# Performance work log

Hardware: AMD Instinct MI355X
Metric: run time of the kernel (lower is better)

Reference implementation:

```python
import jax, jax.numpy as jnp
import numpy as np

N, E, F_IN, F_OUT, K = 10000, 640000, 256, 64, 4


def setup_inputs() -> dict:
    key = jax.random.key(0)
    ks = jax.random.split(key, 8)
    feat = jax.random.normal(ks[0], (N, F_IN), dtype=jnp.float32)
    feat_a = jax.random.normal(ks[1], (N, F_IN), dtype=jnp.float32)
    edge_index = jax.random.randint(ks[2], (2, E), 0, N)
    graph_neigh = jax.random.uniform(ks[3], (N, N), dtype=jnp.float32)
    W = jax.random.normal(ks[4], ((K + 1) * F_IN, F_OUT), dtype=jnp.float32) * 0.05
    Wb = jax.random.normal(ks[5], (F_OUT, F_OUT), dtype=jnp.float32) * 0.05
    b = jnp.zeros((), dtype=jnp.float32)
    return {"feat": feat, "feat_a": feat_a, "edge_index": edge_index,
            "graph_neigh": graph_neigh, "W": W, "Wb": Wb, "b": b}


def _sym_norm(edge_index, num_nodes):
    # add_remaining_self_loops with all-ones weights: drop existing self-loops,
    # append a weight-1 self loop per node (fill_value=1, improved=False)
    row, col = edge_index[0], edge_index[1]
    w = jnp.where(row == col, 0.0, 1.0).astype(jnp.float32)
    loop = jnp.arange(num_nodes)
    row = jnp.concatenate([row, loop])
    col = jnp.concatenate([col, loop])
    w = jnp.concatenate([w, jnp.ones((num_nodes,), jnp.float32)])
    deg = jax.ops.segment_sum(w, row, num_segments=num_nodes)
    dis = jnp.where(deg > 0, jax.lax.rsqrt(deg), 0.0)  # inf -> 0
    norm = dis[row] * w * dis[col]
    return row, col, norm


def _comb_unweighted(x, row, col, norm, k_hops):
    # K-hop propagation: out[dst] += norm * x[src]; concat hops 0..K
    xs = [x]
    for _ in range(k_hops):
        msg = norm[:, None] * xs[-1][row]          # gather + scale  [E', F]
        xs.append(jax.ops.segment_sum(msg, col, num_segments=x.shape[0]))
    return jnp.concatenate(xs, axis=1)             # [N, F*(K+1)]


def _avg_readout(emb, mask):
    vsum = mask @ emb                              # [N, F_OUT]
    row_sum = jnp.sum(mask, axis=1, keepdims=True)
    g = vsum / row_sum
    nrm = jnp.linalg.norm(g, axis=1, keepdims=True)
    return g / jnp.maximum(nrm, 1e-12)             # F.normalize p=2


def _disc(c, h_pl, h_mi, Wb, b):
    # nn.Bilinear(n_h, n_h, 1): sc = h^T Wb c + b, per node
    sc1 = jnp.einsum('nd,de,ne->n', h_pl, Wb, c) + b
    sc2 = jnp.einsum('nd,de,ne->n', h_mi, Wb, c) + b
    return jnp.stack([sc1, sc2], axis=1)           # [N, 2]


def reference(feat, feat_a, edge_index, graph_neigh, W, Wb, b):
    row, col, norm = _sym_norm(edge_index, feat.shape[0])
    h = _comb_unweighted(feat, row, col, norm, K) @ W
    h_a = _comb_unweighted(feat_a, row, col, norm, K) @ W
    emb = jax.nn.relu(h)
    emb_a = jax.nn.relu(h_a)
    g = jax.nn.sigmoid(_avg_readout(emb, graph_neigh))
    g_a = jax.nn.sigmoid(_avg_readout(emb_a, graph_neigh))
    ret = _disc(g, emb, emb_a, Wb, b)
    ret_a = _disc(g_a, emb_a, emb, Wb, b)
    return emb, ret, ret_a
```

## Files before the change

kernel.cpp:

```cpp
#include <hip/hip_runtime.h>
#include <hip/hip_bf16.h>
#include <hip/hip_fp16.h>

typedef float f32x4 __attribute__((ext_vector_type(4)));
typedef short s16x8 __attribute__((ext_vector_type(8)));
typedef unsigned int u32x4 __attribute__((ext_vector_type(4)));

#define F_IN 256
#define F_OUT 64
#define KSPLIT 13
#define HBLK 80

static __device__ __forceinline__ short f2bf(float f){
  union { float f; unsigned u; } x; x.f = f;
  unsigned r = (x.u + 0x7FFFu + ((x.u >> 16) & 1u)) >> 16;
  return (short)r;
}

static __device__ __forceinline__ unsigned pack_rtne(float f0, float f1){
  return ((unsigned)(unsigned short)f2bf(f0)) | ((unsigned)(unsigned short)f2bf(f1) << 16);
}

static __device__ __forceinline__ unsigned pack_trunc(float f0, float f1){
  return (__float_as_uint(f0) >> 16) | (__float_as_uint(f1) & 0xFFFF0000u);
}

static __device__ __forceinline__ float bf_lo(unsigned u){ return __uint_as_float(u << 16); }
static __device__ __forceinline__ float bf_hi(unsigned u){ return __uint_as_float(u & 0xFFFF0000u); }
static __device__ __forceinline__ float h16(unsigned u){
  return __half2float(__ushort_as_half((unsigned short)(u >> 16)));
}

union FragU { u32x4 u; s16x8 s; };


__global__ void wt_zero_kernel(const float* __restrict__ W, short* __restrict__ WT,
                               int* __restrict__ deg, int* __restrict__ counts, int n){
  int idx = blockIdx.x * blockDim.x + threadIdx.x;
  if (idx < n){ deg[idx] = 0; counts[idx] = 0; }
  if (idx < 5 * 64 * 256){
    int k = idx & 255, c = (idx >> 8) & 63, by = idx >> 14;
    WT[idx] = f2bf(W[(size_t)(by * 256 + k) * 64 + c]);
  }
}


__global__ __launch_bounds__(1024) void hist_kernel(const int* __restrict__ ei, int E,
                                                    int* __restrict__ deg,
                                                    int* __restrict__ counts,
                                                    int* __restrict__ blkcnt, int n){
  __shared__ int bins[10240];
  int tid = threadIdx.x;
  int per = (E + HBLK - 1) / HBLK;
  int e0 = blockIdx.x * per, e1 = min(E, e0 + per);

  for (int i = tid; i < n; i += 1024) bins[i] = 0;
  __syncthreads();
  for (int e = e0 + tid; e < e1; e += 1024){
    int r = ei[e], c = ei[E + e];
    if (r != c) atomicAdd(&bins[c], 1);
  }
  __syncthreads();
  for (int i = tid; i < n; i += 1024){
    int v = bins[i];
    blkcnt[(size_t)blockIdx.x * n + i] = v;
    if (v) atomicAdd(&counts[i], v);
  }
  __syncthreads();

  for (int i = tid; i < n; i += 1024) bins[i] = 0;
  __syncthreads();
  for (int e = e0 + tid; e < e1; e += 1024){
    int r = ei[e], c = ei[E + e];
    if (r != c) atomicAdd(&bins[r], 1);
  }
  __syncthreads();
  for (int i = tid; i < n; i += 1024){ int v = bins[i]; if (v) atomicAdd(&deg[i], v); }
}


__global__ __launch_bounds__(1024) void scan_kernel(const int* __restrict__ counts,
                                                    const int* __restrict__ deg,
                                                    float* __restrict__ dis,
                                                    float* __restrict__ selfnorm,
                                                    int* __restrict__ offsets, int n){
  const int C = 10;
  __shared__ int vals[10240];
  __shared__ int wsum[1024];
  int tid = threadIdx.x;
  for (int i = tid; i < 10240; i += 1024) vals[i] = (i < n) ? counts[i] : 0;
  for (int i = tid; i < n; i += 1024){
    float d = (float)(deg[i] + 1);
    dis[i] = rsqrtf(d);
    selfnorm[i] = 1.0f / d;
  }
  __syncthreads();
  int base = tid * C;
  int s = 0;
  #pragma unroll
  for (int i = 0; i < C; ++i) s += vals[base + i];
  wsum[tid] = s; __syncthreads();
  for (int off = 1; off < 1024; off <<= 1){
    int add = (tid >= off) ? wsum[tid - off] : 0;
    __syncthreads();
    wsum[tid] += add;
    __syncthreads();
  }
  int run = wsum[tid] - s;
  #pragma unroll
  for (int i = 0; i < C; ++i){ int v = vals[base + i]; vals[base + i] = run; run += v; }
  __syncthreads();
  for (int i = tid; i < 10240; i += 1024)
    if (i < n) offsets[i] = vals[i];
  if (tid == 1023) offsets[n] = wsum[1023];
}


__global__ void blkbase_kernel(const int* __restrict__ offsets, const int* __restrict__ blkcnt,
                               int* __restrict__ blkbase, int n){
  int bin = blockIdx.x * blockDim.x + threadIdx.x;
  if (bin >= n) return;
  int run = offsets[bin];
  for (int blk = 0; blk < HBLK; ++blk){
    blkbase[(size_t)blk * n + bin] = run;
    run += blkcnt[(size_t)blk * n + bin];
  }
}


__global__ __launch_bounds__(1024) void fill_kernel(const int* __restrict__ ei, int E,
                                                    const float* __restrict__ dis,
                                                    const int* __restrict__ blkbase,
                                                    unsigned* __restrict__ csr, int n){
  __shared__ int bins[10240];
  int tid = threadIdx.x;
  int per = (E + HBLK - 1) / HBLK;
  int e0 = blockIdx.x * per, e1 = min(E, e0 + per);
  for (int i = tid; i < n; i += 1024) bins[i] = blkbase[(size_t)blockIdx.x * n + i];
  __syncthreads();
  for (int e = e0 + tid; e < e1; e += 1024){
    int r = ei[e], c = ei[E + e];
    if (r == c) continue;
    int pos = atomicAdd(&bins[c], 1);
    unsigned h = (unsigned)__half_as_ushort(__float2half(dis[r] * dis[c]));
    csr[pos] = (unsigned)r | (h << 16);
  }
}


__global__ __launch_bounds__(64) void fgemm_kernel(const float* __restrict__ X0,
                                                   const float* __restrict__ X1,
                                                   const short* __restrict__ WT,
                                                   float* __restrict__ Yc,
                                                   short* __restrict__ t0bf, int M){
  int bz = blockIdx.y;
  const float* X = bz ? X1 : X0;
  int l = threadIdx.x, lr = l & 15, g = l >> 4;
  int row0 = blockIdx.x * 16;
  const f32x4* ap = (const f32x4*)(X + (size_t)(row0 + lr) * F_IN + g * 8);
  s16x8 afr[8];
  #pragma unroll
  for (int it = 0; it < 8; ++it){
    f32x4 x0 = ap[it * 8], x1 = ap[it * 8 + 1];
    FragU af;
    af.u[0] = pack_rtne(x0[0], x0[1]); af.u[1] = pack_rtne(x0[2], x0[3]);
    af.u[2] = pack_rtne(x1[0], x1[1]); af.u[3] = pack_rtne(x1[2], x1[3]);
    afr[it] = af.s;
  }
  for (int by = 0; by < 5; ++by){
    f32x4 acc[4];
    #pragma unroll
    for (int ct = 0; ct < 4; ++ct) acc[ct] = (f32x4){0,0,0,0};
    const s16x8* bp[4];
    #pragma unroll
    for (int ct = 0; ct < 4; ++ct)
      bp[ct] = (const s16x8*)(WT + ((size_t)by * 64 + ct * 16 + lr) * F_IN + g * 8);
    #pragma unroll
    for (int it = 0; it < 8; ++it)
      #pragma unroll
      for (int ct = 0; ct < 4; ++ct)
        acc[ct] = __builtin_amdgcn_mfma_f32_16x16x32_bf16(afr[it], bp[ct][it * 4], acc[ct], 0, 0, 0);
    float* yp = Yc + (size_t)by * M * 128 + (size_t)bz * 64;
    #pragma unroll
    for (int ct = 0; ct < 4; ++ct)
      #pragma unroll
      for (int i = 0; i < 4; ++i){
        int grow = row0 + g * 4 + i;
        yp[(size_t)grow * 128 + ct * 16 + lr] = acc[ct][i];
        if (by == 4) t0bf[(size_t)grow * 128 + bz * 64 + ct * 16 + lr] = f2bf(acc[ct][i]);
      }
  }
}


__global__ __launch_bounds__(256) void gather_kernel(const float* __restrict__ Yk,
    const unsigned* __restrict__ tinb, const int* __restrict__ offsets,
    const unsigned* __restrict__ csr, const float* __restrict__ selfnorm,
    unsigned* __restrict__ toutb, float* __restrict__ toutf, int n, int wantf){
  int wid = threadIdx.x >> 6, lane = threadIdx.x & 63;
  int node = blockIdx.x * 4 + wid;
  if (node >= n) return;
  int e0 = offsets[node], e1 = offsets[node + 1];
  float sn = selfnorm[node];
  unsigned t0 = tinb[(size_t)node * 64 + lane];
  float2 yk = ((const float2*)Yk)[(size_t)node * 64 + lane];
  float ax = yk.x + sn * bf_lo(t0);
  float ay = yk.y + sn * bf_hi(t0);
  int i = e0;
  for (; i + 4 <= e1; i += 4){
    unsigned q0 = csr[i], q1 = csr[i+1], q2 = csr[i+2], q3 = csr[i+3];
    float w0 = h16(q0), w1 = h16(q1), w2 = h16(q2), w3 = h16(q3);
    unsigned v0 = tinb[(size_t)(q0 & 0xFFFFu) * 64 + lane];
    unsigned v1 = tinb[(size_t)(q1 & 0xFFFFu) * 64 + lane];
    unsigned v2 = tinb[(size_t)(q2 & 0xFFFFu) * 64 + lane];
    unsigned v3 = tinb[(size_t)(q3 & 0xFFFFu) * 64 + lane];
    ax += w0 * bf_lo(v0); ay += w0 * bf_hi(v0);
    ax += w1 * bf_lo(v1); ay += w1 * bf_hi(v1);
    ax += w2 * bf_lo(v2); ay += w2 * bf_hi(v2);
    ax += w3 * bf_lo(v3); ay += w3 * bf_hi(v3);
  }
  for (; i < e1; ++i){
    unsigned q = csr[i];
    float w = h16(q);
    unsigned v = tinb[(size_t)(q & 0xFFFFu) * 64 + lane];
    ax += w * bf_lo(v); ay += w * bf_hi(v);
  }
  if (wantf){
    float2 r; r.x = ax; r.y = ay;
    ((float2*)toutf)[(size_t)node * 64 + lane] = r;
  } else {
    toutb[(size_t)node * 64 + lane] = pack_rtne(ax, ay);
  }
}


__global__ __launch_bounds__(256) void relu_trans_kernel(const float* __restrict__ u,
    float* __restrict__ emb, float* __restrict__ emb_a, short* __restrict__ embBT, int n){
  __shared__ short lds[128 * 72];
  int t = threadIdx.x;
  int node0 = blockIdx.x * 64;
  int nl = t >> 2;
  int f0 = (t & 3) * 32;
  int node = node0 + nl;
  if (node < n){
    const f32x4* up = (const f32x4*)(u + (size_t)node * 128 + f0);
    float* dst = (f0 < 64) ? (emb + (size_t)node * 64 + f0)
                           : (emb_a + (size_t)node * 64 + (f0 - 64));
    #pragma unroll
    for (int j4 = 0; j4 < 8; ++j4){
      f32x4 v = up[j4];
      #pragma unroll
      for (int e = 0; e < 4; ++e){
        float x = v[e] > 0.0f ? v[e] : 0.0f;
        v[e] = x;
        lds[(f0 + j4 * 4 + e) * 72 + nl] = f2bf(x);
      }
      ((f32x4*)dst)[j4] = v;
    }
  }
  __syncthreads();
  int f = t >> 1, c0 = (t & 1) * 32;
  short* op = embBT + (size_t)f * n + node0 + c0;
  const short* lp = lds + f * 72 + c0;
  if (node0 + 64 <= n){
    #pragma unroll
    for (int j = 0; j < 4; ++j)
      *(s16x8*)(op + j * 8) = *(const s16x8*)(lp + j * 8);
  } else {
    for (int j = 0; j < 32; ++j)
      if (node0 + c0 + j < n) op[j] = lp[j];
  }
}


__global__ __launch_bounds__(256, 4) void readout_kernel(const float* __restrict__ mask,
    const short* __restrict__ embBT, float* __restrict__ vsum, int n){
  __shared__ float Ab[2][64][32];
  __shared__ short Bb[2][128][32];
  int t = threadIdx.x;
  int w = t >> 6, l = t & 63, lr = l & 15, g = l >> 4;
  int row0 = blockIdx.x * 64;
  int ks = blockIdx.y;

  int steps_total = (n + 31) >> 5;
  int per = steps_total / KSPLIT, rem = steps_total % KSPLIT;
  int sbeg = ks * per + (ks < rem ? ks : rem);
  int scnt = per + (ks < rem ? 1 : 0);
  bool tail = ((sbeg + scnt) == steps_total) && ((n & 31) != 0);
  int nf = scnt - (tail ? 1 : 0);
  int kb0 = sbeg << 5;

  int arow = row0 + w * 16 + (l >> 3);
  int aswz = ((l & 7) ^ ((l >> 3) & 7)) << 2;
  const float* asrc0 = mask + (size_t)min(arow,     n - 1) * n + aswz;
  const float* asrc1 = mask + (size_t)min(arow + 8, n - 1) * n + aswz;
  int bcol = w * 32 + (l >> 2);
  int bswz = ((l & 3) ^ ((l >> 3) & 3)) << 3;
  const short* bsrc0 = embBT + (size_t)bcol * n + bswz;
  const short* bsrc1 = embBT + (size_t)(bcol + 16) * n + bswz;

  #define GLDS(gp, lp) __builtin_amdgcn_global_load_lds( \
      (const __attribute__((address_space(1))) void*)(const void*)(gp), \
      (__attribute__((address_space(3))) void*)(void*)(lp), 16, 0, 0)
  #define STAGE(kb, bi) do{ \
    GLDS(asrc0 + (kb), &Ab[bi][w * 16     ][0]); \
    GLDS(asrc1 + (kb), &Ab[bi][w * 16 +  8][0]); \
    GLDS(bsrc0 + (kb), &Bb[bi][w * 32     ][0]); \
    GLDS(bsrc1 + (kb), &Bb[bi][w * 32 + 16][0]); \
  }while(0)

  f32x4 acc[8];
  #pragma unroll
  for (int ct = 0; ct < 8; ++ct) acc[ct] = (f32x4){0,0,0,0};

  if (nf > 0) STAGE(kb0, 0);
  if (nf > 1) STAGE(kb0 + 32, 1);

  for (int s = 0; s < nf; ++s){
    if (s + 1 < nf) asm volatile("s_waitcnt vmcnt(4)" ::: "memory");
    else            asm volatile("s_waitcnt vmcnt(0)" ::: "memory");
    __builtin_amdgcn_s_barrier();
    int cur = s & 1;
    f32x4 x0 = *(const f32x4*)&Ab[cur][w * 16 + lr][((2 * g)     ^ (lr & 7)) << 2];
    f32x4 x1 = *(const f32x4*)&Ab[cur][w * 16 + lr][((2 * g + 1) ^ (lr & 7)) << 2];
    FragU af;
    af.u[0] = pack_trunc(x0[0], x0[1]); af.u[1] = pack_trunc(x0[2], x0[3]);
    af.u[2] = pack_trunc(x1[0], x1[1]); af.u[3] = pack_trunc(x1[2], x1[3]);
    #pragma unroll
    for (int ct = 0; ct < 8; ++ct){
      s16x8 bf = *(const s16x8*)&Bb[cur][ct * 16 + lr][(g ^ ((lr >> 1) & 3)) << 3];
      acc[ct] = __builtin_amdgcn_mfma_f32_16x16x32_bf16(af.s, bf, acc[ct], 0, 0, 0);
    }
    asm volatile("s_waitcnt lgkmcnt(0)" ::: "memory");
    __builtin_amdgcn_s_barrier();
    if (s + 2 < nf) STAGE(kb0 + (s + 2) * 32, cur);
  }
  #undef STAGE
  #undef GLDS

  if (tail){
    int kb = kb0 + nf * 32;
    int kleft = n - kb;
    FragU af; af.u = (u32x4){0,0,0,0};
    const s16x8 bz = {0,0,0,0,0,0,0,0};
    s16x8 bf[8];
    #pragma unroll
    for (int ct = 0; ct < 8; ++ct) bf[ct] = bz;
    int r = row0 + w * 16 + lr;
    if (g * 8 < kleft){
      if (r < n){
        const f32x4* p = (const f32x4*)(mask + (size_t)r * n + kb + g * 8);
        f32x4 r0 = p[0], r1 = p[1];
        af.u[0] = pack_trunc(r0[0], r0[1]); af.u[1] = pack_trunc(r0[2], r0[3]);
        af.u[2] = pack_trunc(r1[0], r1[1]); af.u[3] = pack_trunc(r1[2], r1[3]);
      }
      #pragma unroll
      for (int ct = 0; ct < 8; ++ct)
        bf[ct] = *(const s16x8*)(embBT + (size_t)(ct * 16 + lr) * n + kb + g * 8);
    }
    #pragma unroll
    for (int ct = 0; ct < 8; ++ct)
      acc[ct] = __builtin_amdgcn_mfma_f32_16x16x32_bf16(af.s, bf[ct], acc[ct], 0, 0, 0);
  }

  float* vs = vsum + (size_t)ks * n * 128;
  int rbase = row0 + w * 16;
  #pragma unroll
  for (int ct = 0; ct < 8; ++ct)
    #pragma unroll
    for (int i = 0; i < 4; ++i){
      int gr = rbase + g * 4 + i;
      if (gr < n) vs[(size_t)gr * 128 + ct * 16 + lr] = acc[ct][i];
    }
}


__global__ __launch_bounds__(256) void gnorm_disc_kernel(const float* __restrict__ vsum,
    const float* __restrict__ emb, const float* __restrict__ emb_a,
    const float* __restrict__ Wb, const float* __restrict__ bptr,
    float* __restrict__ ret, float* __restrict__ reta, int n){
  __shared__ float Wl[64][65];
  int t = threadIdx.x;
  for (int i = t; i < 4096; i += 256) Wl[i >> 6][i & 63] = Wb[i];
  __syncthreads();
  int wid = t >> 6, lane = t & 63;
  int node = blockIdx.x * 4 + wid;
  if (node >= n) return;

  size_t stride = (size_t)n * 128;
  float v1 = 0.0f, v2 = 0.0f;
  #pragma unroll
  for (int ks = 0; ks < KSPLIT; ++ks){
    v1 += vsum[ks * stride + (size_t)node * 128 + lane];
    v2 += vsum[ks * stride + (size_t)node * 128 + 64 + lane];
  }
  float s1 = v1 * v1, s2 = v2 * v2;
  for (int off = 32; off >= 1; off >>= 1){
    s1 += __shfl_xor(s1, off);
    s2 += __shfl_xor(s2, off);
  }
  float i1 = v1 / fmaxf(sqrtf(s1), 1e-12f);
  float i2 = v2 / fmaxf(sqrtf(s2), 1e-12f);
  float g1 = 1.0f / (1.0f + expf(-i1));
  float g2 = 1.0f / (1.0f + expf(-i2));

  float e1 = emb[(size_t)node * 64 + lane];
  float e2 = emb_a[(size_t)node * 64 + lane];
  float u1 = 0.0f, u2 = 0.0f;
  for (int e = 0; e < 64; ++e){
    float wv = Wl[lane][e];
    u1 += wv * __shfl(g1, e);
    u2 += wv * __shfl(g2, e);
  }
  float p1 = e1 * u1, p2 = e2 * u1, p3 = e2 * u2, p4 = e1 * u2;
  for (int off = 32; off >= 1; off >>= 1){
    p1 += __shfl_xor(p1, off); p2 += __shfl_xor(p2, off);
    p3 += __shfl_xor(p3, off); p4 += __shfl_xor(p4, off);
  }
  if (lane == 0){
    float b = bptr[0];
    ret[(size_t)node * 2 + 0]  = p1 + b;
    ret[(size_t)node * 2 + 1]  = p2 + b;
    reta[(size_t)node * 2 + 0] = p3 + b;
    reta[(size_t)node * 2 + 1] = p4 + b;
  }
}


extern "C" void kernel_launch(void* const* d_in, const int* in_sizes, int n_in,
                              void* d_out, int out_size, void* d_ws, size_t ws_size,
                              hipStream_t stream) {
  const float* feat   = (const float*)d_in[0];
  const float* feat_a = (const float*)d_in[1];
  const int*   ei     = (const int*)d_in[2];
  const float* mask   = (const float*)d_in[3];
  const float* W      = (const float*)d_in[4];
  const float* Wb     = (const float*)d_in[5];
  const float* bsc    = (const float*)d_in[6];
  const int n = in_sizes[0] / F_IN;
  const int E = in_sizes[2] / 2;
  const size_t sl128 = (size_t)n * 128;

  float* out  = (float*)d_out;
  float* ret  = out + (size_t)n * F_OUT;
  float* reta = ret + (size_t)n * 2;

  char* wsb = (char*)d_ws;
  size_t off = 0;
  #define WSALLOC(ptr, T, cnt) T* ptr = (T*)(wsb + off); off = (off + sizeof(T)*(size_t)(cnt) + 255) & ~(size_t)255
  WSALLOC(deg, int, n);
  WSALLOC(counts, int, n);
  WSALLOC(offs, int, n + 1);
  WSALLOC(dis, float, n);
  WSALLOC(selfnorm, float, n);
  WSALLOC(csr, unsigned, E);
  WSALLOC(blkcnt, int, (size_t)HBLK * n);
  WSALLOC(blkbase, int, (size_t)HBLK * n);
  WSALLOC(WT, short, 5 * 64 * 256);
  WSALLOC(Yc, float, sl128 * 5);
  WSALLOC(t0bf, unsigned, (size_t)n * 64);
  WSALLOC(tb0, unsigned, (size_t)n * 64);
  WSALLOC(tb1, unsigned, (size_t)n * 64);
  WSALLOC(u1, float, sl128);
  WSALLOC(emb_a, float, (size_t)n * F_OUT);
  WSALLOC(embBT, short, (size_t)128 * n);
  WSALLOC(vsum, float, sl128 * KSPLIT);
  (void)ws_size; (void)n_in; (void)out_size;

  wt_zero_kernel<<<(5 * 64 * 256 + 255) / 256, 256, 0, stream>>>(W, WT, deg, counts, n);
  hist_kernel<<<HBLK, 1024, 0, stream>>>(ei, E, deg, counts, blkcnt, n);
  scan_kernel<<<1, 1024, 0, stream>>>(counts, deg, dis, selfnorm, offs, n);
  blkbase_kernel<<<(n + 255) / 256, 256, 0, stream>>>(offs, blkcnt, blkbase, n);
  fill_kernel<<<HBLK, 1024, 0, stream>>>(ei, E, dis, blkbase, csr, n);

  fgemm_kernel<<<dim3(n / 16, 2), 64, 0, stream>>>(feat, feat_a, WT, Yc, (short*)t0bf, n);

  int gb = (n + 3) / 4;
  gather_kernel<<<gb, 256, 0, stream>>>(Yc + 3 * sl128, t0bf, offs, csr, selfnorm, tb0, (float*)0, n, 0);
  gather_kernel<<<gb, 256, 0, stream>>>(Yc + 2 * sl128, tb0,  offs, csr, selfnorm, tb1, (float*)0, n, 0);
  gather_kernel<<<gb, 256, 0, stream>>>(Yc + 1 * sl128, tb1,  offs, csr, selfnorm, tb0, (float*)0, n, 0);
  gather_kernel<<<gb, 256, 0, stream>>>(Yc + 0 * sl128, tb0,  offs, csr, selfnorm, (unsigned*)0, u1, n, 1);
  relu_trans_kernel<<<(n + 63) / 64, 256, 0, stream>>>(u1, out, emb_a, embBT, n);

  readout_kernel<<<dim3((n + 63) / 64, KSPLIT), 256, 0, stream>>>(mask, embBT, vsum, n);
  gnorm_disc_kernel<<<gb, 256, 0, stream>>>(vsum, out, emb_a, Wb, bsc, ret, reta, n);
}
```

Measured before the change: 358.9 us.

## Enlarge readout tile to 128 rows, retune split-K and histogram block count

The readout GEMM (mask @ emb) now computes 128 rows per block, each wave holding two 16-row tiles and reusing the same B fragments from LDS for both. This halves how often embBT is reloaded per mask row and raises MFMA work per barrier, at the cost of more registers and LDS (occupancy hint lowered to 3). KSPLIT drops from 13 to 9 to keep the grid size reasonable, and the histogram/fill block count rises to 240, which gives more parallelism there but makes the blkbase scan loop longer (it is unrolled by 8).

```diff
diff --git a/kernel.cpp b/kernel.cpp
--- a/kernel.cpp
+++ b/kernel.cpp
@@ -8,8 +8,8 @@
 
 #define F_IN 256
 #define F_OUT 64
-#define KSPLIT 13
-#define HBLK 80
+#define KSPLIT 9
+#define HBLK 240
 
 static __device__ __forceinline__ short f2bf(float f){
   union { float f; unsigned u; } x; x.f = f;
@@ -121,6 +121,7 @@
   int bin = blockIdx.x * blockDim.x + threadIdx.x;
   if (bin >= n) return;
   int run = offsets[bin];
+  #pragma unroll 8
   for (int blk = 0; blk < HBLK; ++blk){
     blkbase[(size_t)blk * n + bin] = run;
     run += blkcnt[(size_t)blk * n + bin];
@@ -273,13 +274,13 @@
 }
 
 
-__global__ __launch_bounds__(256, 4) void readout_kernel(const float* __restrict__ mask,
+__global__ __launch_bounds__(256, 3) void readout_kernel(const float* __restrict__ mask,
     const short* __restrict__ embBT, float* __restrict__ vsum, int n){
-  __shared__ float Ab[2][64][32];
+  __shared__ float Ab[2][128][32];
   __shared__ short Bb[2][128][32];
   int t = threadIdx.x;
   int w = t >> 6, l = t & 63, lr = l & 15, g = l >> 4;
-  int row0 = blockIdx.x * 64;
+  int row0 = blockIdx.x * 128;
   int ks = blockIdx.y;
 
   int steps_total = (n + 31) >> 5;
@@ -290,10 +291,13 @@
   int nf = scnt - (tail ? 1 : 0);
   int kb0 = sbeg << 5;
 
-  int arow = row0 + w * 16 + (l >> 3);
   int aswz = ((l & 7) ^ ((l >> 3) & 7)) << 2;
-  const float* asrc0 = mask + (size_t)min(arow,     n - 1) * n + aswz;
-  const float* asrc1 = mask + (size_t)min(arow + 8, n - 1) * n + aswz;
+  const float* asrc[4];
+  #pragma unroll
+  for (int j = 0; j < 4; ++j){
+    int ar = row0 + w * 32 + j * 8 + (l >> 3);
+    asrc[j] = mask + (size_t)min(ar, n - 1) * n + aswz;
+  }
   int bcol = w * 32 + (l >> 2);
   int bswz = ((l & 3) ^ ((l >> 3) & 3)) << 3;
   const short* bsrc0 = embBT + (size_t)bcol * n + bswz;
@@ -303,33 +307,42 @@
       (const __attribute__((address_space(1))) void*)(const void*)(gp), \
       (__attribute__((address_space(3))) void*)(void*)(lp), 16, 0, 0)
   #define STAGE(kb, bi) do{ \
-    GLDS(asrc0 + (kb), &Ab[bi][w * 16     ][0]); \
-    GLDS(asrc1 + (kb), &Ab[bi][w * 16 +  8][0]); \
+    GLDS(asrc[0] + (kb), &Ab[bi][w * 32     ][0]); \
+    GLDS(asrc[1] + (kb), &Ab[bi][w * 32 +  8][0]); \
+    GLDS(asrc[2] + (kb), &Ab[bi][w * 32 + 16][0]); \
+    GLDS(asrc[3] + (kb), &Ab[bi][w * 32 + 24][0]); \
     GLDS(bsrc0 + (kb), &Bb[bi][w * 32     ][0]); \
     GLDS(bsrc1 + (kb), &Bb[bi][w * 32 + 16][0]); \
   }while(0)
 
-  f32x4 acc[8];
-  #pragma unroll
-  for (int ct = 0; ct < 8; ++ct) acc[ct] = (f32x4){0,0,0,0};
+  f32x4 acc[2][8];
+  #pragma unroll
+  for (int rt = 0; rt < 2; ++rt)
+    #pragma unroll
+    for (int ct = 0; ct < 8; ++ct) acc[rt][ct] = (f32x4){0,0,0,0};
 
   if (nf > 0) STAGE(kb0, 0);
   if (nf > 1) STAGE(kb0 + 32, 1);
 
   for (int s = 0; s < nf; ++s){
-    if (s + 1 < nf) asm volatile("s_waitcnt vmcnt(4)" ::: "memory");
+    if (s + 1 < nf) asm volatile("s_waitcnt vmcnt(6)" ::: "memory");
     else            asm volatile("s_waitcnt vmcnt(0)" ::: "memory");
     __builtin_amdgcn_s_barrier();
     int cur = s & 1;
-    f32x4 x0 = *(const f32x4*)&Ab[cur][w * 16 + lr][((2 * g)     ^ (lr & 7)) << 2];
-    f32x4 x1 = *(const f32x4*)&Ab[cur][w * 16 + lr][((2 * g + 1) ^ (lr & 7)) << 2];
-    FragU af;
-    af.u[0] = pack_trunc(x0[0], x0[1]); af.u[1] = pack_trunc(x0[2], x0[3]);
-    af.u[2] = pack_trunc(x1[0], x1[1]); af.u[3] = pack_trunc(x1[2], x1[3]);
-    #pragma unroll
-    for (int ct = 0; ct < 8; ++ct){
-      s16x8 bf = *(const s16x8*)&Bb[cur][ct * 16 + lr][(g ^ ((lr >> 1) & 3)) << 3];
-      acc[ct] = __builtin_amdgcn_mfma_f32_16x16x32_bf16(af.s, bf, acc[ct], 0, 0, 0);
+    s16x8 bfr[8];
+    #pragma unroll
+    for (int ct = 0; ct < 8; ++ct)
+      bfr[ct] = *(const s16x8*)&Bb[cur][ct * 16 + lr][(g ^ ((lr >> 1) & 3)) << 3];
+    #pragma unroll
+    for (int rt = 0; rt < 2; ++rt){
+      f32x4 x0 = *(const f32x4*)&Ab[cur][w * 32 + rt * 16 + lr][((2 * g)     ^ (lr & 7)) << 2];
+      f32x4 x1 = *(const f32x4*)&Ab[cur][w * 32 + rt * 16 + lr][((2 * g + 1) ^ (lr & 7)) << 2];
+      FragU af;
+      af.u[0] = pack_trunc(x0[0], x0[1]); af.u[1] = pack_trunc(x0[2], x0[3]);
+      af.u[2] = pack_trunc(x1[0], x1[1]); af.u[3] = pack_trunc(x1[2], x1[3]);
+      #pragma unroll
+      for (int ct = 0; ct < 8; ++ct)
+        acc[rt][ct] = __builtin_amdgcn_mfma_f32_16x16x32_bf16(af.s, bfr[ct], acc[rt][ct], 0, 0, 0);
     }
     asm volatile("s_waitcnt lgkmcnt(0)" ::: "memory");
     __builtin_amdgcn_s_barrier();
@@ -341,14 +354,16 @@
   if (tail){
     int kb = kb0 + nf * 32;
     int kleft = n - kb;
-    FragU af; af.u = (u32x4){0,0,0,0};
     const s16x8 bz = {0,0,0,0,0,0,0,0};
-    s16x8 bf[8];
-    #pragma unroll
-    for (int ct = 0; ct < 8; ++ct) bf[ct] = bz;
-    int r = row0 + w * 16 + lr;
-    if (g * 8 < kleft){
-      if (r < n){
+    s16x8 bfr[8];
+    #pragma unroll
+    for (int ct = 0; ct < 8; ++ct)
+      bfr[ct] = (g * 8 < kleft) ? *(const s16x8*)(embBT + (size_t)(ct * 16 + lr) * n + kb + g * 8) : bz;
+    #pragma unroll
+    for (int rt = 0; rt < 2; ++rt){
+      FragU af; af.u = (u32x4){0,0,0,0};
+      int r = row0 + w * 32 + rt * 16 + lr;
+      if (g * 8 < kleft && r < n){
         const f32x4* p = (const f32x4*)(mask + (size_t)r * n + kb + g * 8);
         f32x4 r0 = p[0], r1 = p[1];
         af.u[0] = pack_trunc(r0[0], r0[1]); af.u[1] = pack_trunc(r0[2], r0[3]);
@@ -356,22 +371,22 @@
       }
       #pragma unroll
       for (int ct = 0; ct < 8; ++ct)
-        bf[ct] = *(const s16x8*)(embBT + (size_t)(ct * 16 + lr) * n + kb + g * 8);
+        acc[rt][ct] = __builtin_amdgcn_mfma_f32_16x16x32_bf16(af.s, bfr[ct], acc[rt][ct], 0, 0, 0);
     }
+  }
+
+  float* vs = vsum + (size_t)ks * n * 128;
+  #pragma unroll
+  for (int rt = 0; rt < 2; ++rt){
+    int rbase = row0 + w * 32 + rt * 16;
     #pragma unroll
     for (int ct = 0; ct < 8; ++ct)
-      acc[ct] = __builtin_amdgcn_mfma_f32_16x16x32_bf16(af.s, bf[ct], acc[ct], 0, 0, 0);
-  }
-
-  float* vs = vsum + (size_t)ks * n * 128;
-  int rbase = row0 + w * 16;
-  #pragma unroll
-  for (int ct = 0; ct < 8; ++ct)
-    #pragma unroll
-    for (int i = 0; i < 4; ++i){
-      int gr = rbase + g * 4 + i;
-      if (gr < n) vs[(size_t)gr * 128 + ct * 16 + lr] = acc[ct][i];
-    }
+      #pragma unroll
+      for (int i = 0; i < 4; ++i){
+        int gr = rbase + g * 4 + i;
+        if (gr < n) vs[(size_t)gr * 128 + ct * 16 + lr] = acc[rt][ct][i];
+      }
+  }
 }
 
 
@@ -482,6 +497,6 @@
   gather_kernel<<<gb, 256, 0, stream>>>(Yc + 0 * sl128, tb0,  offs, csr, selfnorm, (unsigned*)0, u1, n, 1);
   relu_trans_kernel<<<(n + 63) / 64, 256, 0, stream>>>(u1, out, emb_a, embBT, n);
 
-  readout_kernel<<<dim3((n + 63) / 64, KSPLIT), 256, 0, stream>>>(mask, embBT, vsum, n);
+  readout_kernel<<<dim3((n + 127) / 128, KSPLIT), 256, 0, stream>>>(mask, embBT, vsum, n);
   gnorm_disc_kernel<<<gb, 256, 0, stream>>>(vsum, out, emb_a, Wb, bsc, ret, reta, n);
 }
```

New measurement: 343.4 us. 4.3% less time.
